# Optimization experiments

Hardware: AMD Instinct MI355X
Metric: run time of the kernel (lower is better)

Reference implementation:

```python
import jax, jax.numpy as jnp
import numpy as np

N_NODES = 100000
N_EDGES = 600000
EMB_DIM = 128
N_BOND_FEATS = 3
BOND_VOCAB = 8


def setup_inputs() -> dict:
    key = jax.random.key(0)
    k1, k2, k3, k4, k5, k6 = jax.random.split(key, 6)
    h = jax.random.normal(k1, (N_NODES, EMB_DIM), dtype=jnp.float32)
    edge_feat = jax.random.randint(k2, (N_EDGES, N_BOND_FEATS), 0, 5, dtype=jnp.int64)
    dst = jax.random.randint(k3, (N_EDGES,), 0, N_NODES, dtype=jnp.int64)
    bond_emb = jax.random.normal(k4, (N_BOND_FEATS, BOND_VOCAB, EMB_DIM), dtype=jnp.float32)
    W = jax.random.normal(k5, (EMB_DIM, EMB_DIM), dtype=jnp.float32) / jnp.sqrt(jnp.float32(EMB_DIM))
    b = jax.random.normal(k6, (EMB_DIM,), dtype=jnp.float32) * 0.01
    return {"h": h, "edge_feat": edge_feat, "dst": dst, "bond_emb": bond_emb, "W": W, "b": b}


def reference(h, edge_feat, dst, bond_emb, W, b):
    # BondEncoder: sum of per-column embedding lookups -> [E, D]
    # bond_emb[f, edge_feat[:, f]] for each feature column f, summed.
    he = bond_emb[jnp.arange(N_BOND_FEATS)[None, :], edge_feat].sum(axis=1)  # [E, D]
    # fn.v_mul_e: message = dst-node feature * encoded edge feature
    m = h[dst] * he  # [E, D]
    # fn.sum: segment-sum messages onto destination nodes
    agg = jax.ops.segment_sum(m, dst, num_segments=N_NODES)  # [N, D]
    # final Linear(emb_dim, emb_dim)
    return agg @ W.T + b
```

## Files before the change

### kernel.cpp

```cpp
#include <hip/hip_runtime.h>

#define NN 100000
#define NE 600000
#define D 128
#define CW 16

#define OFF_CNTBF  6400000
#define OFF_WSPLIT 9600000
#define OFF_EFRAG  9665536

typedef __attribute__((ext_vector_type(8))) short bf16x8;
typedef __attribute__((ext_vector_type(4))) float f32x4;

__device__ __forceinline__ unsigned short f2bf(float x) {
    unsigned u = __float_as_uint(x);
    u += 0x7FFFu + ((u >> 16) & 1u);
    return (unsigned short)(u >> 16);
}
__device__ __forceinline__ float bf2f(unsigned short s) {
    return __uint_as_float(((unsigned)s) << 16);
}
__device__ __forceinline__ unsigned pack2(unsigned short a, unsigned short b) {
    return (unsigned)a | ((unsigned)b << 16);
}

__global__ __launch_bounds__(256) void prep_kernel(const float* __restrict__ W,
                                                   const float* __restrict__ emb,
                                                   unsigned char* __restrict__ ws) {
    int bid = blockIdx.x;
    if (bid < 1563) {
        int c = bid * 256 + threadIdx.x;
        if (c < 400000) reinterpret_cast<int4*>(ws)[c] = make_int4(0, 0, 0, 0);
    } else if (bid < 1627) {
        int idx = (bid - 1563) * 256 + threadIdx.x;
        float w = W[idx];
        unsigned short hi = f2bf(w);
        unsigned short lo = f2bf(w - bf2f(hi));
        unsigned short* wsplit = (unsigned short*)(ws + OFF_WSPLIT);
        wsplit[idx] = hi;
        wsplit[16384 + idx] = lo;
    } else {
        int i = (bid - 1627) * 256 + threadIdx.x;
        int e = i & 7, l = (i >> 3) & 63, t = (i >> 9) & 7;
        int r = l & 15, lg = l >> 4;
        int j = lg * 8 + e;
        int d = 32 * (t >> 1) + 8 * (r >> 2) + 4 * (t & 1) + (r & 3);
        float v = 0.0f;
        if (j < 15) v = emb[((j / 5) * 8 + (j % 5)) * D + d];
        unsigned short hi = f2bf(v);
        unsigned short lo = f2bf(v - bf2f(hi));
        unsigned short* ef = (unsigned short*)(ws + OFF_EFRAG);
        ef[i] = hi;
        ef[4096 + i] = lo;
    }
}

__global__ __launch_bounds__(256) void hist_kernel(const int* __restrict__ ef,
                                                   const int* __restrict__ dst,
                                                   unsigned* __restrict__ counts) {
    int g = blockIdx.x * 256 + threadIdx.x;
    if (g >= NE / 4) return;
    int4 d4 = reinterpret_cast<const int4*>(dst)[g];
    int4 f0 = reinterpret_cast<const int4*>(ef)[g * 3 + 0];
    int4 f1 = reinterpret_cast<const int4*>(ef)[g * 3 + 1];
    int4 f2 = reinterpret_cast<const int4*>(ef)[g * 3 + 2];
    int fa[12] = {f0.x, f0.y, f0.z, f0.w, f1.x, f1.y, f1.z, f1.w,
                  f2.x, f2.y, f2.z, f2.w};
    int dd[4] = {d4.x, d4.y, d4.z, d4.w};
    #pragma unroll
    for (int i = 0; i < 4; ++i) {
        int combo = fa[i * 3] * 25 + fa[i * 3 + 1] * 5 + fa[i * 3 + 2];
        atomicAdd(counts + dd[i] * CW + (combo >> 3), 1u << ((combo & 7) * 4));
    }
}

__global__ __launch_bounds__(256) void expand_kernel(const unsigned* __restrict__ counts,
                                                     unsigned short* __restrict__ cntbf) {
    int n = blockIdx.x * 256 + threadIdx.x;
    if (n >= NN) return;
    const unsigned* row = counts + n * CW;
    unsigned wd[16];
    #pragma unroll
    for (int i = 0; i < 4; ++i) {
        uint4 v = reinterpret_cast<const uint4*>(row)[i];
        wd[i * 4] = v.x; wd[i * 4 + 1] = v.y; wd[i * 4 + 2] = v.z; wd[i * 4 + 3] = v.w;
    }
    int mi[15];
    #pragma unroll
    for (int j = 0; j < 15; ++j) mi[j] = 0;
    #pragma unroll
    for (int c = 0; c < 125; ++c) {
        int cnt = (int)((wd[c >> 3] >> ((c & 7) * 4)) & 0xFu);
        mi[c / 25] += cnt;
        mi[5 + (c / 5) % 5] += cnt;
        mi[10 + c % 5] += cnt;
    }
    unsigned short o[16];
    #pragma unroll
    for (int j = 0; j < 15; ++j) o[j] = f2bf((float)mi[j]);
    o[15] = 0;
    uint4 u;
    u.x = pack2(o[0], o[1]);   u.y = pack2(o[2], o[3]);
    u.z = pack2(o[4], o[5]);   u.w = pack2(o[6], o[7]);
    reinterpret_cast<uint4*>(cntbf + n * 16)[0] = u;
    u.x = pack2(o[8], o[9]);   u.y = pack2(o[10], o[11]);
    u.z = pack2(o[12], o[13]); u.w = pack2(o[14], o[15]);
    reinterpret_cast<uint4*>(cntbf + n * 16)[1] = u;
}

__global__ __launch_bounds__(512, 4) void fused_kernel(
        const float* __restrict__ h,
        const unsigned short* __restrict__ cntbf,
        const unsigned short* __restrict__ efrag,
        const unsigned short* __restrict__ wsplit,
        const float* __restrict__ b,
        float* __restrict__ out) {
    __shared__ unsigned short sW[2][128 * 128];

    const int tid  = threadIdx.x;
    const int lane = tid & 63;
    const int w    = tid >> 6;
    const int n0   = blockIdx.x * 128;
    const int lr   = lane & 15;
    const int lg   = lane >> 4;

    char* sWb = (char*)&sW[0][0];

    #pragma unroll
    for (int i = 0; i < 8; ++i) {
        int c  = tid + i * 512;
        int p  = c >> 11;
        int r  = (c >> 4) & 127;
        int kc = c & 15;
        int byte = p * 32768 + r * 256 + ((kc * 16) ^ ((r & 7) << 4));
        *reinterpret_cast<uint4*>(sWb + byte) = reinterpret_cast<const uint4*>(wsplit)[c];
    }

    const int node  = n0 + w * 16 + lr;
    const bool valid = node < NN;

    float hv[4][8];
    #pragma unroll
    for (int kk = 0; kk < 4; ++kk) {
        if (valid) {
            float4 h0 = *reinterpret_cast<const float4*>(h + node * D + kk * 32 + lg * 8);
            float4 h1 = *reinterpret_cast<const float4*>(h + node * D + kk * 32 + lg * 8 + 4);
            hv[kk][0] = h0.x; hv[kk][1] = h0.y; hv[kk][2] = h0.z; hv[kk][3] = h0.w;
            hv[kk][4] = h1.x; hv[kk][5] = h1.y; hv[kk][6] = h1.z; hv[kk][7] = h1.w;
        } else {
            #pragma unroll
            for (int e = 0; e < 8; ++e) hv[kk][e] = 0.0f;
        }
    }

    bf16x8 cfrag = {0, 0, 0, 0, 0, 0, 0, 0};
    if (valid && lg < 2)
        cfrag = *reinterpret_cast<const bf16x8*>(cntbf + node * 16 + lg * 8);

    f32x4 s[8];
    #pragma unroll
    for (int t = 0; t < 8; ++t) { f32x4 z = {0, 0, 0, 0}; s[t] = z; }
    #pragma unroll
    for (int p = 0; p < 2; ++p) {
        #pragma unroll
        for (int t = 0; t < 8; ++t) {
            bf16x8 ef = *reinterpret_cast<const bf16x8*>(efrag + p * 4096 + t * 512 + lane * 8);
            s[t] = __builtin_amdgcn_mfma_f32_16x16x32_bf16(ef, cfrag, s[t], 0, 0, 0);
        }
    }

    bf16x8 afrag[4];
    #pragma unroll
    for (int kk = 0; kk < 4; ++kk) {
        unsigned short o[8];
        #pragma unroll
        for (int e = 0; e < 8; ++e)
            o[e] = f2bf(hv[kk][e] * s[kk * 2 + (e >> 2)][e & 3]);
        unsigned uo[4];
        uo[0] = pack2(o[0], o[1]); uo[1] = pack2(o[2], o[3]);
        uo[2] = pack2(o[4], o[5]); uo[3] = pack2(o[6], o[7]);
        afrag[kk] = *reinterpret_cast<bf16x8*>(uo);
    }
    __syncthreads();

    f32x4 acc[8];
    #pragma unroll
    for (int jb = 0; jb < 8; ++jb) {
        float bv = b[jb * 16 + lr];
        f32x4 t = {bv, bv, bv, bv};
        acc[jb] = t;
    }

    #pragma unroll
    for (int kk = 0; kk < 4; ++kk) {
        #pragma unroll
        for (int jb = 0; jb < 8; ++jb) {
            int brow  = jb * 16 + lr;
            int wbyte = brow * 256 + ((kk * 64 + lg * 16) ^ ((brow & 7) << 4));
            bf16x8 whi = *reinterpret_cast<const bf16x8*>(sWb + wbyte);
            bf16x8 wlo = *reinterpret_cast<const bf16x8*>(sWb + 32768 + wbyte);
            acc[jb] = __builtin_amdgcn_mfma_f32_16x16x32_bf16(afrag[kk], whi, acc[jb], 0, 0, 0);
            acc[jb] = __builtin_amdgcn_mfma_f32_16x16x32_bf16(afrag[kk], wlo, acc[jb], 0, 0, 0);
        }
    }

    #pragma unroll
    for (int jb = 0; jb < 8; ++jb) {
        int col = jb * 16 + lr;
        #pragma unroll
        for (int r = 0; r < 4; ++r) {
            int n2 = n0 + w * 16 + lg * 4 + r;
            if (n2 < NN) out[n2 * D + col] = acc[jb][r];
        }
    }
}

extern "C" void kernel_launch(void* const* d_in, const int* in_sizes, int n_in,
                              void* d_out, int out_size, void* d_ws, size_t ws_size,
                              hipStream_t stream) {
    const float* h   = (const float*)d_in[0];
    const int*   ef  = (const int*)d_in[1];
    const int*   dst = (const int*)d_in[2];
    const float* emb = (const float*)d_in[3];
    const float* W   = (const float*)d_in[4];
    const float* b   = (const float*)d_in[5];
    float*       out = (float*)d_out;

    unsigned char*  ws     = (unsigned char*)d_ws;
    unsigned*       counts = (unsigned*)ws;
    unsigned short* cntbf  = (unsigned short*)(ws + OFF_CNTBF);
    unsigned short* wsplit = (unsigned short*)(ws + OFF_WSPLIT);
    unsigned short* efr    = (unsigned short*)(ws + OFF_EFRAG);

    prep_kernel<<<1563 + 64 + 16, 256, 0, stream>>>(W, emb, ws);
    hist_kernel<<<(NE / 4 + 255) / 256, 256, 0, stream>>>(ef, dst, counts);
    expand_kernel<<<(NN + 255) / 256, 256, 0, stream>>>(counts, cntbf);
    fused_kernel<<<(NN + 127) / 128, 512, 0, stream>>>(h, cntbf, efr, wsplit, b, out);
}
```

Before: 63.53 us.

## Stage activations in LDS and read W fragments from global per wave tile

The fused kernel no longer copies the split bf16 W (64KB) into shared memory per block. Instead each wave writes its scaled activation fragments to a 32KB shared buffer, and after the barrier computes a 64-node by 32-column output tile. B fragments are loaded directly from global memory (L2/L1-cached) and A fragments are reused from LDS. This halves LDS use and removes the per-block W staging traffic, which may raise occupancy. The cost is global W loads inside the MFMA loop and more scattered output stores.

Measured after the change: 73.26 us. +15.3%, slower.

```diff
diff --git a/kernel.cpp b/kernel.cpp
--- a/kernel.cpp
+++ b/kernel.cpp
@@ -115,7 +115,7 @@
         const unsigned short* __restrict__ wsplit,
         const float* __restrict__ b,
         float* __restrict__ out) {
-    __shared__ unsigned short sW[2][128 * 128];
+    __shared__ unsigned short sA[128 * 128];
 
     const int tid  = threadIdx.x;
     const int lane = tid & 63;
@@ -123,18 +123,7 @@
     const int n0   = blockIdx.x * 128;
     const int lr   = lane & 15;
     const int lg   = lane >> 4;
-
-    char* sWb = (char*)&sW[0][0];
-
-    #pragma unroll
-    for (int i = 0; i < 8; ++i) {
-        int c  = tid + i * 512;
-        int p  = c >> 11;
-        int r  = (c >> 4) & 127;
-        int kc = c & 15;
-        int byte = p * 32768 + r * 256 + ((kc * 16) ^ ((r & 7) << 4));
-        *reinterpret_cast<uint4*>(sWb + byte) = reinterpret_cast<const uint4*>(wsplit)[c];
-    }
+    char* sAb = (char*)sA;
 
     const int node  = n0 + w * 16 + lr;
     const bool valid = node < NN;
@@ -169,48 +158,66 @@
         }
     }
 
-    bf16x8 afrag[4];
     #pragma unroll
     for (int kk = 0; kk < 4; ++kk) {
         unsigned short o[8];
         #pragma unroll
         for (int e = 0; e < 8; ++e)
             o[e] = f2bf(hv[kk][e] * s[kk * 2 + (e >> 2)][e & 3]);
-        unsigned uo[4];
-        uo[0] = pack2(o[0], o[1]); uo[1] = pack2(o[2], o[3]);
-        uo[2] = pack2(o[4], o[5]); uo[3] = pack2(o[6], o[7]);
-        afrag[kk] = *reinterpret_cast<bf16x8*>(uo);
+        uint4 uo;
+        uo.x = pack2(o[0], o[1]); uo.y = pack2(o[2], o[3]);
+        uo.z = pack2(o[4], o[5]); uo.w = pack2(o[6], o[7]);
+        *reinterpret_cast<uint4*>(sAb + w * 4096 + kk * 1024 + lane * 16) = uo;
     }
     __syncthreads();
 
-    f32x4 acc[8];
-    #pragma unroll
-    for (int jb = 0; jb < 8; ++jb) {
-        float bv = b[jb * 16 + lr];
+    const int nh = w >> 2;
+    const int cq = w & 3;
+
+    f32x4 acc[4][2];
+    #pragma unroll
+    for (int j = 0; j < 2; ++j) {
+        float bv = b[cq * 32 + j * 16 + lr];
         f32x4 t = {bv, bv, bv, bv};
-        acc[jb] = t;
+        #pragma unroll
+        for (int i = 0; i < 4; ++i) acc[i][j] = t;
     }
 
     #pragma unroll
     for (int kk = 0; kk < 4; ++kk) {
-        #pragma unroll
-        for (int jb = 0; jb < 8; ++jb) {
-            int brow  = jb * 16 + lr;
-            int wbyte = brow * 256 + ((kk * 64 + lg * 16) ^ ((brow & 7) << 4));
-            bf16x8 whi = *reinterpret_cast<const bf16x8*>(sWb + wbyte);
-            bf16x8 wlo = *reinterpret_cast<const bf16x8*>(sWb + 32768 + wbyte);
-            acc[jb] = __builtin_amdgcn_mfma_f32_16x16x32_bf16(afrag[kk], whi, acc[jb], 0, 0, 0);
-            acc[jb] = __builtin_amdgcn_mfma_f32_16x16x32_bf16(afrag[kk], wlo, acc[jb], 0, 0, 0);
-        }
-    }
-
-    #pragma unroll
-    for (int jb = 0; jb < 8; ++jb) {
-        int col = jb * 16 + lr;
-        #pragma unroll
-        for (int r = 0; r < 4; ++r) {
-            int n2 = n0 + w * 16 + lg * 4 + r;
-            if (n2 < NN) out[n2 * D + col] = acc[jb][r];
+        bf16x8 bh[2], bl[2];
+        #pragma unroll
+        for (int j = 0; j < 2; ++j) {
+            int col = cq * 32 + j * 16 + lr;
+            const unsigned short* bp = wsplit + col * 128 + kk * 32 + lg * 8;
+            bh[j] = *reinterpret_cast<const bf16x8*>(bp);
+            bl[j] = *reinterpret_cast<const bf16x8*>(bp + 16384);
+        }
+        bf16x8 a[4];
+        #pragma unroll
+        for (int i = 0; i < 4; ++i)
+            a[i] = *reinterpret_cast<const bf16x8*>(
+                sAb + (nh * 4 + i) * 4096 + kk * 1024 + lane * 16);
+        #pragma unroll
+        for (int i = 0; i < 4; ++i) {
+            #pragma unroll
+            for (int j = 0; j < 2; ++j) {
+                acc[i][j] = __builtin_amdgcn_mfma_f32_16x16x32_bf16(a[i], bh[j], acc[i][j], 0, 0, 0);
+                acc[i][j] = __builtin_amdgcn_mfma_f32_16x16x32_bf16(a[i], bl[j], acc[i][j], 0, 0, 0);
+            }
+        }
+    }
+
+    #pragma unroll
+    for (int i = 0; i < 4; ++i) {
+        #pragma unroll
+        for (int j = 0; j < 2; ++j) {
+            int col = cq * 32 + j * 16 + lr;
+            #pragma unroll
+            for (int r = 0; r < 4; ++r) {
+                int n2 = n0 + nh * 64 + i * 16 + lg * 4 + r;
+                if (n2 < NN) out[n2 * D + col] = acc[i][j][r];
+            }
         }
     }
 }
```

## Drop LDS staging of split W; read it from global per wave and simplify histogram

Applied to the files above, without the earlier changes.

The fused kernel no longer copies the hi/lo bf16 split weights into shared memory with a block-wide barrier. Each wave now works independently on 16 nodes and reads W fragments straight from global memory (64 KB, likely L1/L2 resident). Blocks shrink to 256 threads, and the h loads are interleaved with the scaling step. The histogram kernel moves from four edges per thread with int4 loads to one edge per thread with scalar loads. The intent is to remove LDS fill and sync overhead and raise occupancy, at the cost of more global or cache traffic for W and less vectorized histogram loads.

After: 107.3 us. +68.9%, slower.

```diff
diff --git a/kernel.cpp b/kernel.cpp
--- a/kernel.cpp
+++ b/kernel.cpp
@@ -58,20 +58,14 @@
 __global__ __launch_bounds__(256) void hist_kernel(const int* __restrict__ ef,
                                                    const int* __restrict__ dst,
                                                    unsigned* __restrict__ counts) {
-    int g = blockIdx.x * 256 + threadIdx.x;
-    if (g >= NE / 4) return;
-    int4 d4 = reinterpret_cast<const int4*>(dst)[g];
-    int4 f0 = reinterpret_cast<const int4*>(ef)[g * 3 + 0];
-    int4 f1 = reinterpret_cast<const int4*>(ef)[g * 3 + 1];
-    int4 f2 = reinterpret_cast<const int4*>(ef)[g * 3 + 2];
-    int fa[12] = {f0.x, f0.y, f0.z, f0.w, f1.x, f1.y, f1.z, f1.w,
-                  f2.x, f2.y, f2.z, f2.w};
-    int dd[4] = {d4.x, d4.y, d4.z, d4.w};
-    #pragma unroll
-    for (int i = 0; i < 4; ++i) {
-        int combo = fa[i * 3] * 25 + fa[i * 3 + 1] * 5 + fa[i * 3 + 2];
-        atomicAdd(counts + dd[i] * CW + (combo >> 3), 1u << ((combo & 7) * 4));
-    }
+    int e = blockIdx.x * 256 + threadIdx.x;
+    if (e >= NE) return;
+    int n  = dst[e];
+    int f0 = ef[e * 3 + 0];
+    int f1 = ef[e * 3 + 1];
+    int f2 = ef[e * 3 + 2];
+    int combo = f0 * 25 + f1 * 5 + f2;
+    atomicAdd(counts + n * CW + (combo >> 3), 1u << ((combo & 7) * 4));
 }
 
 __global__ __launch_bounds__(256) void expand_kernel(const unsigned* __restrict__ counts,
@@ -108,80 +102,59 @@
     reinterpret_cast<uint4*>(cntbf + n * 16)[1] = u;
 }
 
-__global__ __launch_bounds__(512, 4) void fused_kernel(
+__global__ __launch_bounds__(256, 4) void fused_kernel(
         const float* __restrict__ h,
         const unsigned short* __restrict__ cntbf,
         const unsigned short* __restrict__ efrag,
         const unsigned short* __restrict__ wsplit,
         const float* __restrict__ b,
         float* __restrict__ out) {
-    __shared__ unsigned short sW[2][128 * 128];
-
-    const int tid  = threadIdx.x;
-    const int lane = tid & 63;
-    const int w    = tid >> 6;
-    const int n0   = blockIdx.x * 128;
+    const int lane = threadIdx.x & 63;
+    const int wid  = (blockIdx.x * 256 + threadIdx.x) >> 6;
+    if (wid >= (NN + 15) / 16) return;
     const int lr   = lane & 15;
     const int lg   = lane >> 4;
-
-    char* sWb = (char*)&sW[0][0];
-
-    #pragma unroll
-    for (int i = 0; i < 8; ++i) {
-        int c  = tid + i * 512;
-        int p  = c >> 11;
-        int r  = (c >> 4) & 127;
-        int kc = c & 15;
-        int byte = p * 32768 + r * 256 + ((kc * 16) ^ ((r & 7) << 4));
-        *reinterpret_cast<uint4*>(sWb + byte) = reinterpret_cast<const uint4*>(wsplit)[c];
-    }
-
-    const int node  = n0 + w * 16 + lr;
+    const int node = wid * 16 + lr;
     const bool valid = node < NN;
 
-    float hv[4][8];
+    bf16x8 cfrag = {0, 0, 0, 0, 0, 0, 0, 0};
+    if (valid && lg < 2)
+        cfrag = *reinterpret_cast<const bf16x8*>(cntbf + node * 16 + lg * 8);
+
+    f32x4 s[8];
+    #pragma unroll
+    for (int t = 0; t < 8; ++t) { f32x4 z = {0, 0, 0, 0}; s[t] = z; }
+    #pragma unroll
+    for (int p = 0; p < 2; ++p) {
+        #pragma unroll
+        for (int t = 0; t < 8; ++t) {
+            bf16x8 ef = *reinterpret_cast<const bf16x8*>(efrag + p * 4096 + t * 512 + lane * 8);
+            s[t] = __builtin_amdgcn_mfma_f32_16x16x32_bf16(ef, cfrag, s[t], 0, 0, 0);
+        }
+    }
+
+    bf16x8 afrag[4];
     #pragma unroll
     for (int kk = 0; kk < 4; ++kk) {
+        float hv[8];
         if (valid) {
             float4 h0 = *reinterpret_cast<const float4*>(h + node * D + kk * 32 + lg * 8);
             float4 h1 = *reinterpret_cast<const float4*>(h + node * D + kk * 32 + lg * 8 + 4);
-            hv[kk][0] = h0.x; hv[kk][1] = h0.y; hv[kk][2] = h0.z; hv[kk][3] = h0.w;
-            hv[kk][4] = h1.x; hv[kk][5] = h1.y; hv[kk][6] = h1.z; hv[kk][7] = h1.w;
+            hv[0] = h0.x; hv[1] = h0.y; hv[2] = h0.z; hv[3] = h0.w;
+            hv[4] = h1.x; hv[5] = h1.y; hv[6] = h1.z; hv[7] = h1.w;
         } else {
             #pragma unroll
-            for (int e = 0; e < 8; ++e) hv[kk][e] = 0.0f;
-        }
-    }
-
-    bf16x8 cfrag = {0, 0, 0, 0, 0, 0, 0, 0};
-    if (valid && lg < 2)
-        cfrag = *reinterpret_cast<const bf16x8*>(cntbf + node * 16 + lg * 8);
-
-    f32x4 s[8];
-    #pragma unroll
-    for (int t = 0; t < 8; ++t) { f32x4 z = {0, 0, 0, 0}; s[t] = z; }
-    #pragma unroll
-    for (int p = 0; p < 2; ++p) {
-        #pragma unroll
-        for (int t = 0; t < 8; ++t) {
-            bf16x8 ef = *reinterpret_cast<const bf16x8*>(efrag + p * 4096 + t * 512 + lane * 8);
-            s[t] = __builtin_amdgcn_mfma_f32_16x16x32_bf16(ef, cfrag, s[t], 0, 0, 0);
-        }
-    }
-
-    bf16x8 afrag[4];
-    #pragma unroll
-    for (int kk = 0; kk < 4; ++kk) {
+            for (int e = 0; e < 8; ++e) hv[e] = 0.0f;
+        }
         unsigned short o[8];
         #pragma unroll
         for (int e = 0; e < 8; ++e)
-            o[e] = f2bf(hv[kk][e] * s[kk * 2 + (e >> 2)][e & 3]);
+            o[e] = f2bf(hv[e] * s[kk * 2 + (e >> 2)][e & 3]);
         unsigned uo[4];
         uo[0] = pack2(o[0], o[1]); uo[1] = pack2(o[2], o[3]);
         uo[2] = pack2(o[4], o[5]); uo[3] = pack2(o[6], o[7]);
         afrag[kk] = *reinterpret_cast<bf16x8*>(uo);
     }
-    __syncthreads();
 
     f32x4 acc[8];
     #pragma unroll
@@ -192,15 +165,14 @@
     }
 
     #pragma unroll
-    for (int kk = 0; kk < 4; ++kk) {
-        #pragma unroll
-        for (int jb = 0; jb < 8; ++jb) {
-            int brow  = jb * 16 + lr;
-            int wbyte = brow * 256 + ((kk * 64 + lg * 16) ^ ((brow & 7) << 4));
-            bf16x8 whi = *reinterpret_cast<const bf16x8*>(sWb + wbyte);
-            bf16x8 wlo = *reinterpret_cast<const bf16x8*>(sWb + 32768 + wbyte);
-            acc[jb] = __builtin_amdgcn_mfma_f32_16x16x32_bf16(afrag[kk], whi, acc[jb], 0, 0, 0);
-            acc[jb] = __builtin_amdgcn_mfma_f32_16x16x32_bf16(afrag[kk], wlo, acc[jb], 0, 0, 0);
+    for (int jb = 0; jb < 8; ++jb) {
+        #pragma unroll
+        for (int kk = 0; kk < 4; ++kk) {
+            const unsigned short* bp = wsplit + (jb * 16 + lr) * 128 + kk * 32 + lg * 8;
+            bf16x8 bh = *reinterpret_cast<const bf16x8*>(bp);
+            bf16x8 bl = *reinterpret_cast<const bf16x8*>(bp + 16384);
+            acc[jb] = __builtin_amdgcn_mfma_f32_16x16x32_bf16(afrag[kk], bh, acc[jb], 0, 0, 0);
+            acc[jb] = __builtin_amdgcn_mfma_f32_16x16x32_bf16(afrag[kk], bl, acc[jb], 0, 0, 0);
         }
     }
 
@@ -209,7 +181,7 @@
         int col = jb * 16 + lr;
         #pragma unroll
         for (int r = 0; r < 4; ++r) {
-            int n2 = n0 + w * 16 + lg * 4 + r;
+            int n2 = wid * 16 + lg * 4 + r;
             if (n2 < NN) out[n2 * D + col] = acc[jb][r];
         }
     }
@@ -233,7 +205,8 @@
     unsigned short* efr    = (unsigned short*)(ws + OFF_EFRAG);
 
     prep_kernel<<<1563 + 64 + 16, 256, 0, stream>>>(W, emb, ws);
-    hist_kernel<<<(NE / 4 + 255) / 256, 256, 0, stream>>>(ef, dst, counts);
+    hist_kernel<<<(NE + 255) / 256, 256, 0, stream>>>(ef, dst, counts);
     expand_kernel<<<(NN + 255) / 256, 256, 0, stream>>>(counts, cntbf);
-    fused_kernel<<<(NN + 127) / 128, 512, 0, stream>>>(h, cntbf, efr, wsplit, b, out);
-}
+    int nwaves = (NN + 15) / 16;
+    fused_kernel<<<(nwaves + 3) / 4, 256, 0, stream>>>(h, cntbf, efr, wsplit, b, out);
+}
```

## Load W fragments directly from global into registers, drop LDS staging

Applied to the files above, without the earlier changes.

The fused kernel no longer stages the split bf16 weight matrix in shared memory with a block-wide barrier. Each wave now reads its B fragments straight from global memory, through the caches, into double-buffered registers, and interleaves those loads with the MFMA chain. Blocks shrink to 256 threads and each wave handles 16 nodes on its own. This removes the 64KB LDS footprint and the barrier so more blocks can be resident, at the cost of much higher register pressure (64 bf16x8 buffers) and repeated L2 reads of W by every wave.

Result: slower. 106.1 us (+67.1%).

```diff
diff --git a/kernel.cpp b/kernel.cpp
--- a/kernel.cpp
+++ b/kernel.cpp
@@ -108,36 +108,43 @@
     reinterpret_cast<uint4*>(cntbf + n * 16)[1] = u;
 }
 
-__global__ __launch_bounds__(512, 4) void fused_kernel(
+#define LOADB(BUF, KK)                                                         \
+    _Pragma("unroll")                                                          \
+    for (int jb = 0; jb < 8; ++jb) {                                           \
+        const unsigned short* bp = wsplit + (jb * 16 + lr) * 128 + (KK) * 32 + lg * 8; \
+        BUF##h[jb] = *reinterpret_cast<const bf16x8*>(bp);                     \
+        BUF##l[jb] = *reinterpret_cast<const bf16x8*>(bp + 16384);             \
+    }
+
+#define MMAB(BUF, AF)                                                          \
+    _Pragma("unroll")                                                          \
+    for (int jb = 0; jb < 8; ++jb) {                                           \
+        acc[jb] = __builtin_amdgcn_mfma_f32_16x16x32_bf16(AF, BUF##h[jb], acc[jb], 0, 0, 0); \
+        acc[jb] = __builtin_amdgcn_mfma_f32_16x16x32_bf16(AF, BUF##l[jb], acc[jb], 0, 0, 0); \
+    }
+
+__global__ __launch_bounds__(256) void fused_kernel(
         const float* __restrict__ h,
         const unsigned short* __restrict__ cntbf,
         const unsigned short* __restrict__ efrag,
         const unsigned short* __restrict__ wsplit,
         const float* __restrict__ b,
         float* __restrict__ out) {
-    __shared__ unsigned short sW[2][128 * 128];
-
-    const int tid  = threadIdx.x;
-    const int lane = tid & 63;
-    const int w    = tid >> 6;
-    const int n0   = blockIdx.x * 128;
+    const int lane = threadIdx.x & 63;
+    const int wid  = (blockIdx.x * 256 + threadIdx.x) >> 6;
+    if (wid >= (NN + 15) / 16) return;
     const int lr   = lane & 15;
     const int lg   = lane >> 4;
-
-    char* sWb = (char*)&sW[0][0];
-
-    #pragma unroll
-    for (int i = 0; i < 8; ++i) {
-        int c  = tid + i * 512;
-        int p  = c >> 11;
-        int r  = (c >> 4) & 127;
-        int kc = c & 15;
-        int byte = p * 32768 + r * 256 + ((kc * 16) ^ ((r & 7) << 4));
-        *reinterpret_cast<uint4*>(sWb + byte) = reinterpret_cast<const uint4*>(wsplit)[c];
-    }
-
-    const int node  = n0 + w * 16 + lr;
+    const int node = wid * 16 + lr;
     const bool valid = node < NN;
+
+    bf16x8 b0h[8], b0l[8], b1h[8], b1l[8];
+
+    LOADB(b0, 0)
+
+    bf16x8 cfrag = {0, 0, 0, 0, 0, 0, 0, 0};
+    if (valid && lg < 2)
+        cfrag = *reinterpret_cast<const bf16x8*>(cntbf + node * 16 + lg * 8);
 
     float hv[4][8];
     #pragma unroll
@@ -153,10 +160,6 @@
         }
     }
 
-    bf16x8 cfrag = {0, 0, 0, 0, 0, 0, 0, 0};
-    if (valid && lg < 2)
-        cfrag = *reinterpret_cast<const bf16x8*>(cntbf + node * 16 + lg * 8);
-
     f32x4 s[8];
     #pragma unroll
     for (int t = 0; t < 8; ++t) { f32x4 z = {0, 0, 0, 0}; s[t] = z; }
@@ -181,7 +184,6 @@
         uo[2] = pack2(o[4], o[5]); uo[3] = pack2(o[6], o[7]);
         afrag[kk] = *reinterpret_cast<bf16x8*>(uo);
     }
-    __syncthreads();
 
     f32x4 acc[8];
     #pragma unroll
@@ -191,25 +193,20 @@
         acc[jb] = t;
     }
 
-    #pragma unroll
-    for (int kk = 0; kk < 4; ++kk) {
-        #pragma unroll
-        for (int jb = 0; jb < 8; ++jb) {
-            int brow  = jb * 16 + lr;
-            int wbyte = brow * 256 + ((kk * 64 + lg * 16) ^ ((brow & 7) << 4));
-            bf16x8 whi = *reinterpret_cast<const bf16x8*>(sWb + wbyte);
-            bf16x8 wlo = *reinterpret_cast<const bf16x8*>(sWb + 32768 + wbyte);
-            acc[jb] = __builtin_amdgcn_mfma_f32_16x16x32_bf16(afrag[kk], whi, acc[jb], 0, 0, 0);
-            acc[jb] = __builtin_amdgcn_mfma_f32_16x16x32_bf16(afrag[kk], wlo, acc[jb], 0, 0, 0);
-        }
-    }
+    LOADB(b1, 1)
+    MMAB(b0, afrag[0])
+    LOADB(b0, 2)
+    MMAB(b1, afrag[1])
+    LOADB(b1, 3)
+    MMAB(b0, afrag[2])
+    MMAB(b1, afrag[3])
 
     #pragma unroll
     for (int jb = 0; jb < 8; ++jb) {
         int col = jb * 16 + lr;
         #pragma unroll
         for (int r = 0; r < 4; ++r) {
-            int n2 = n0 + w * 16 + lg * 4 + r;
+            int n2 = wid * 16 + lg * 4 + r;
             if (n2 < NN) out[n2 * D + col] = acc[jb][r];
         }
     }
@@ -235,5 +232,6 @@
     prep_kernel<<<1563 + 64 + 16, 256, 0, stream>>>(W, emb, ws);
     hist_kernel<<<(NE / 4 + 255) / 256, 256, 0, stream>>>(ef, dst, counts);
     expand_kernel<<<(NN + 255) / 256, 256, 0, stream>>>(counts, cntbf);
-    fused_kernel<<<(NN + 127) / 128, 512, 0, stream>>>(h, cntbf, efr, wsplit, b, out);
-}
+    int nwaves = (NN + 15) / 16;
+    fused_kernel<<<(nwaves + 3) / 4, 256, 0, stream>>>(h, cntbf, efr, wsplit, b, out);
+}
```
